# Kernel tuning notes

Measured on AMD Instinct MI355X. Metric: run time of the kernel, lower is better.

Reference implementation:

```python
import jax, jax.numpy as jnp
import numpy as np


def setup_inputs() -> dict:
    key = jax.random.key(0)
    k1, k2, k3, k4 = jax.random.split(key, 4)
    N, T, F = 8192, 128, 9
    M_s = 256
    merged = jax.random.normal(k1, (N, T, F), dtype=jnp.float32)
    input1 = jax.random.normal(k2, (N, T, F), dtype=jnp.float32)
    samples = jax.random.normal(k3, (N, M_s), dtype=jnp.float32)
    labels = jax.random.randint(k4, (N,), 0, 10, dtype=jnp.int32)
    return {"merged": merged, "input1": input1, "samples": samples, "labels": labels}


def reference(merged, input1, samples, labels):
    # Pairwise squared distances S_ij = sum_k (s_i - s_j)^2 / M_s, computed via
    # the Gram-matrix identity instead of materializing the [N, N, M_s] tensor.
    M_s = samples.shape[1]
    sq = jnp.sum(samples * samples, axis=-1)                 # [N]
    gram = jnp.einsum('im,jm->ij', samples, samples)         # [N, N]
    S_ij = (sq[:, None] + sq[None, :] - 2.0 * gram) / jnp.float32(M_s)
    same = (labels[:, None] == labels[None, :]).astype(jnp.float32)
    term2 = jnp.mean(jnp.maximum(0.0, (1.0 - same) * (1.0 - S_ij)))
    L_label = 10.0 * jnp.mean(same * S_ij) + 10.0 * term2
    return L_label
```

## Files before the change

kernel.cpp:

```cpp
#include <hip/hip_runtime.h>
#include <hip/hip_bf16.h>

#define NROWS 8192
#define KDIM  256
#define NT    64
#define NBLK  (NT * (NT + 1) / 2)
#define GRID  256

typedef __attribute__((ext_vector_type(4))) float f32x4;

#define GLD(gp, lp)                                                            \
  __builtin_amdgcn_global_load_lds(                                            \
      (const __attribute__((address_space(1))) void*)(gp),                     \
      (__attribute__((address_space(3))) void*)(lp), 16, 0, 0)

__global__ void prep_kernel(const float* __restrict__ samples,
                            unsigned char* __restrict__ sf8,
                            float* __restrict__ sq,
                            float* __restrict__ accg) {
  int row = blockIdx.x, t = threadIdx.x;
  float2 v2 = ((const float2*)samples)[(size_t)row * 128 + t];
  int pk = __builtin_amdgcn_cvt_pk_fp8_f32(v2.x, v2.y, 0, false);
  ((unsigned short*)sf8)[(size_t)row * 128 + t] = (unsigned short)(pk & 0xffff);
  float p = v2.x * v2.x + v2.y * v2.y;
#pragma unroll
  for (int off = 32; off; off >>= 1) p += __shfl_down(p, off);
  __shared__ float ws2[2];
  if ((t & 63) == 0) ws2[t >> 6] = p;
  __syncthreads();
  if (t == 0) sq[row] = ws2[0] + ws2[1];
  if (row == 0 && t < 2) accg[t] = 0.0f;
}

__device__ inline void decode_tile(int b, int& bi, int& bj) {
  float disc = (2.0f * NT + 1.0f) * (2.0f * NT + 1.0f) - 8.0f * (float)b;
  bi = (int)(((2.0f * NT + 1.0f) - sqrtf(disc)) * 0.5f);
  if (bi < 0) bi = 0;
  if (bi > NT - 1) bi = NT - 1;
  while (bi > 0 && (bi * NT - bi * (bi - 1) / 2) > b) --bi;
  while (((bi + 1) * NT - (bi + 1) * bi / 2) <= b) ++bi;
  bj = bi + (b - (bi * NT - bi * (bi - 1) / 2));
}

__global__ __launch_bounds__(512, 1) void pair_kernel(
    const unsigned char* __restrict__ sf8, const float* __restrict__ sq,
    const int* __restrict__ labels, float* __restrict__ accg) {

  __shared__ __align__(16) unsigned char As[2][128 * 256];
  __shared__ __align__(16) unsigned char Bs[2][128 * 256];
  __shared__ float red[16];

  int t = threadIdx.x;
  int lane = t & 63;
  int w = t >> 6;
  int wm = w >> 1, wn = w & 1;
  int lr = lane >> 4, pc = lane & 15;
  int r = lane & 15;
  int kq = (lane >> 4) >> 1;
  int hf = ((lane >> 4) & 1) * 8;
  int q4 = (lane >> 4) * 4;
  int cl = lane & 15;

  float s1t = 0.f, s2t = 0.f;

  auto stage = [&](int bi_, int bj_, int buf) {
    int rA = bi_ * 128, rB = bj_ * 128;
#pragma unroll
    for (int p = 0; p < 4; ++p) {
      int region = p * 8 + w;
      int rr = region * 4 + lr;
      int c = pc ^ (rr & 15);
      GLD(sf8 + (size_t)(rA + rr) * KDIM + c * 16, &As[buf][region * 1024]);
      GLD(sf8 + (size_t)(rB + rr) * KDIM + c * 16, &Bs[buf][region * 1024]);
    }
  };

  int tile = blockIdx.x;
  int bi, bj;
  decode_tile(tile, bi, bj);
  stage(bi, bj, 0);
  int cur = 0;

  while (tile < NBLK) {
    int ntile = tile + GRID;
    int nbi = 0, nbj = 0;
    bool have_next = ntile < NBLK;
    if (have_next) decode_tile(ntile, nbi, nbj);

    __syncthreads();

    int rowA0 = bi * 128, rowB0 = bj * 128;
    float sqa[8], sqb[4];
    int laa[8], lab[4];
#pragma unroll
    for (int i = 0; i < 2; i++)
#pragma unroll
      for (int q = 0; q < 4; q++) {
        int gr = rowA0 + wm * 32 + i * 16 + q4 + q;
        sqa[i * 4 + q] = sq[gr];
        laa[i * 4 + q] = labels[gr];
      }
#pragma unroll
    for (int j = 0; j < 4; j++) {
      int gc = rowB0 + wn * 64 + j * 16 + cl;
      sqb[j] = sq[gc];
      lab[j] = labels[gc];
    }

    if (have_next) stage(nbi, nbj, cur ^ 1);

    f32x4 acc[2][4];
#pragma unroll
    for (int i = 0; i < 2; i++)
#pragma unroll
      for (int j = 0; j < 4; j++) acc[i][j] = (f32x4){0.f, 0.f, 0.f, 0.f};

#pragma unroll
    for (int kc = 0; kc < 8; ++kc) {
      long af[2], bfr[4];
#pragma unroll
      for (int i = 0; i < 2; i++) {
        int m = wm * 32 + i * 16 + r;
        af[i] = *(const long*)(&As[cur][m * 256 + (((kc * 2 + kq) ^ r) * 16) + hf]);
      }
#pragma unroll
      for (int j = 0; j < 4; j++) {
        int n = wn * 64 + j * 16 + r;
        bfr[j] = *(const long*)(&Bs[cur][n * 256 + (((kc * 2 + kq) ^ r) * 16) + hf]);
      }
#pragma unroll
      for (int i = 0; i < 2; i++)
#pragma unroll
        for (int j = 0; j < 4; j++)
          acc[i][j] = __builtin_amdgcn_mfma_f32_16x16x32_fp8_fp8(
              af[i], bfr[j], acc[i][j], 0, 0, 0);
    }

    float s1 = 0.f, s2 = 0.f;
#pragma unroll
    for (int j = 0; j < 4; j++) {
#pragma unroll
      for (int i = 0; i < 2; i++) {
#pragma unroll
        for (int q = 0; q < 4; q++) {
          float S = (sqa[i * 4 + q] + sqb[j] - 2.0f * acc[i][j][q]) *
                    (1.0f / 256.0f);
          if (laa[i * 4 + q] == lab[j]) s1 += S;
          else                          s2 += fmaxf(0.f, 1.f - S);
        }
      }
    }
    float wt = (bi == bj) ? 1.0f : 2.0f;
    s1t += wt * s1;
    s2t += wt * s2;

    tile = ntile; bi = nbi; bj = nbj; cur ^= 1;
  }

#pragma unroll
  for (int off = 32; off; off >>= 1) {
    s1t += __shfl_down(s1t, off);
    s2t += __shfl_down(s2t, off);
  }
  if (lane == 0) { red[w] = s1t; red[8 + w] = s2t; }
  __syncthreads();
  if (t == 0) {
    float a = 0.f, b2 = 0.f;
#pragma unroll
    for (int k = 0; k < 8; k++) { a += red[k]; b2 += red[8 + k]; }
    atomicAdd(&accg[0], a);
    atomicAdd(&accg[1], b2);
  }
}

__global__ void finalize_kernel(const float* __restrict__ accg,
                                float* __restrict__ out) {
  out[0] = 10.0f * (accg[0] + accg[1]) *
           (1.0f / ((float)NROWS * (float)NROWS));
}

extern "C" void kernel_launch(void* const* d_in, const int* in_sizes, int n_in,
                              void* d_out, int out_size, void* d_ws,
                              size_t ws_size, hipStream_t stream) {
  const float* samples = (const float*)d_in[2];
  const int*   labels  = (const int*)d_in[3];

  char* ws = (char*)d_ws;
  unsigned char* sf8 = (unsigned char*)ws;
  float* sq   = (float*)(ws + (size_t)NROWS * KDIM);
  float* accg = (float*)(ws + (size_t)NROWS * KDIM + NROWS * 4);
  float* out  = (float*)d_out;

  prep_kernel<<<NROWS, 128, 0, stream>>>(samples, sf8, sq, accg);
  pair_kernel<<<GRID, 512, 0, stream>>>(sf8, sq, labels, accg);
  finalize_kernel<<<1, 1, 0, stream>>>(accg, out);
}
```

Baseline: 136.4 us.

## Switch to 32x32x64 scaled FP8 MFMA with packed row metadata

Replaces the 16x16x32 FP8 MFMA tiles with the gfx950 32x32x64 scaled f8f6f4 MFMA, so each wave issues fewer, larger matrix instructions with 128-bit LDS fragment loads. Squared norms (prescaled by 1/256) and labels are packed into a float2 metadata array in the prep kernel, which cuts the scattered scalar loads in the epilogue. The two loss accumulators are merged into one select-based sum. The accumulator layout changes, so correctness depends on the new lane-to-element mapping being right.

```diff
diff --git a/kernel.cpp b/kernel.cpp
--- a/kernel.cpp
+++ b/kernel.cpp
@@ -1,5 +1,4 @@
 #include <hip/hip_runtime.h>
-#include <hip/hip_bf16.h>
 
 #define NROWS 8192
 #define KDIM  256
@@ -7,7 +6,10 @@
 #define NBLK  (NT * (NT + 1) / 2)
 #define GRID  256
 
-typedef __attribute__((ext_vector_type(4))) float f32x4;
+typedef __attribute__((ext_vector_type(4)))  float f32x4;
+typedef __attribute__((ext_vector_type(16))) float f32x16;
+typedef __attribute__((ext_vector_type(4)))  int   i32x4;
+typedef __attribute__((ext_vector_type(8)))  int   i32x8;
 
 #define GLD(gp, lp)                                                            \
   __builtin_amdgcn_global_load_lds(                                            \
@@ -15,8 +17,9 @@
       (__attribute__((address_space(3))) void*)(lp), 16, 0, 0)
 
 __global__ void prep_kernel(const float* __restrict__ samples,
+                            const int* __restrict__ labels,
                             unsigned char* __restrict__ sf8,
-                            float* __restrict__ sq,
+                            float2* __restrict__ meta,
                             float* __restrict__ accg) {
   int row = blockIdx.x, t = threadIdx.x;
   float2 v2 = ((const float2*)samples)[(size_t)row * 128 + t];
@@ -28,7 +31,10 @@
   __shared__ float ws2[2];
   if ((t & 63) == 0) ws2[t >> 6] = p;
   __syncthreads();
-  if (t == 0) sq[row] = ws2[0] + ws2[1];
+  if (t == 0) {
+    float tot = ws2[0] + ws2[1];
+    meta[row] = make_float2(tot * (1.0f / 256.0f), (float)labels[row]);
+  }
   if (row == 0 && t < 2) accg[t] = 0.0f;
 }
 
@@ -43,25 +49,22 @@
 }
 
 __global__ __launch_bounds__(512, 1) void pair_kernel(
-    const unsigned char* __restrict__ sf8, const float* __restrict__ sq,
-    const int* __restrict__ labels, float* __restrict__ accg) {
+    const unsigned char* __restrict__ sf8, const float2* __restrict__ meta,
+    float* __restrict__ accg) {
 
   __shared__ __align__(16) unsigned char As[2][128 * 256];
   __shared__ __align__(16) unsigned char Bs[2][128 * 256];
-  __shared__ float red[16];
+  __shared__ float red[8];
 
   int t = threadIdx.x;
   int lane = t & 63;
   int w = t >> 6;
   int wm = w >> 1, wn = w & 1;
   int lr = lane >> 4, pc = lane & 15;
-  int r = lane & 15;
-  int kq = (lane >> 4) >> 1;
-  int hf = ((lane >> 4) & 1) * 8;
-  int q4 = (lane >> 4) * 4;
-  int cl = lane & 15;
+  int l31 = lane & 31;
+  int hk  = lane >> 5;
 
-  float s1t = 0.f, s2t = 0.f;
+  float stt = 0.f;
 
   auto stage = [&](int bi_, int bj_, int buf) {
     int rA = bi_ * 128, rB = bj_ * 128;
@@ -90,93 +93,84 @@
     __syncthreads();
 
     int rowA0 = bi * 128, rowB0 = bj * 128;
-    float sqa[8], sqb[4];
-    int laa[8], lab[4];
+    float sqa_s[16], laaf[16];
 #pragma unroll
-    for (int i = 0; i < 2; i++)
+    for (int g = 0; g < 4; ++g) {
+      int gr = rowA0 + wm * 32 + g * 8 + 4 * hk;
+      f32x4 m0 = *(const f32x4*)(meta + gr);
+      f32x4 m1 = *(const f32x4*)(meta + gr + 2);
+      sqa_s[g * 4 + 0] = m0.x; laaf[g * 4 + 0] = m0.y;
+      sqa_s[g * 4 + 1] = m0.z; laaf[g * 4 + 1] = m0.w;
+      sqa_s[g * 4 + 2] = m1.x; laaf[g * 4 + 2] = m1.y;
+      sqa_s[g * 4 + 3] = m1.z; laaf[g * 4 + 3] = m1.w;
+    }
+    float sqb_s[2], labf[2];
 #pragma unroll
-      for (int q = 0; q < 4; q++) {
-        int gr = rowA0 + wm * 32 + i * 16 + q4 + q;
-        sqa[i * 4 + q] = sq[gr];
-        laa[i * 4 + q] = labels[gr];
-      }
-#pragma unroll
-    for (int j = 0; j < 4; j++) {
-      int gc = rowB0 + wn * 64 + j * 16 + cl;
-      sqb[j] = sq[gc];
-      lab[j] = labels[gc];
+    for (int j = 0; j < 2; ++j) {
+      float2 mb = meta[rowB0 + wn * 64 + j * 32 + l31];
+      sqb_s[j] = mb.x; labf[j] = mb.y;
     }
 
     if (have_next) stage(nbi, nbj, cur ^ 1);
 
-    f32x4 acc[2][4];
+    f32x16 acc[2];
 #pragma unroll
-    for (int i = 0; i < 2; i++)
+    for (int j = 0; j < 2; ++j)
 #pragma unroll
-      for (int j = 0; j < 4; j++) acc[i][j] = (f32x4){0.f, 0.f, 0.f, 0.f};
+      for (int e = 0; e < 16; ++e) acc[j][e] = 0.f;
 
 #pragma unroll
-    for (int kc = 0; kc < 8; ++kc) {
-      long af[2], bfr[4];
+    for (int kt = 0; kt < 4; ++kt) {
+      int c0 = kt * 4 + hk * 2;
+      int m = wm * 32 + l31;
+      const unsigned char* ab = &As[cur][m * 256];
+      int sm = m & 15;
+      i32x4 alo = *(const i32x4*)(ab + ((c0 ^ sm) << 4));
+      i32x4 ahi = *(const i32x4*)(ab + (((c0 + 1) ^ sm) << 4));
+      i32x8 av = {alo.x, alo.y, alo.z, alo.w, ahi.x, ahi.y, ahi.z, ahi.w};
 #pragma unroll
-      for (int i = 0; i < 2; i++) {
-        int m = wm * 32 + i * 16 + r;
-        af[i] = *(const long*)(&As[cur][m * 256 + (((kc * 2 + kq) ^ r) * 16) + hf]);
+      for (int j = 0; j < 2; ++j) {
+        int n = wn * 64 + j * 32 + l31;
+        const unsigned char* bb = &Bs[cur][n * 256];
+        int sn = n & 15;
+        i32x4 blo = *(const i32x4*)(bb + ((c0 ^ sn) << 4));
+        i32x4 bhi = *(const i32x4*)(bb + (((c0 + 1) ^ sn) << 4));
+        i32x8 bv = {blo.x, blo.y, blo.z, blo.w, bhi.x, bhi.y, bhi.z, bhi.w};
+        acc[j] = __builtin_amdgcn_mfma_scale_f32_32x32x64_f8f6f4(
+            av, bv, acc[j], 0, 0, 0, 127, 0, 127);
       }
-#pragma unroll
-      for (int j = 0; j < 4; j++) {
-        int n = wn * 64 + j * 16 + r;
-        bfr[j] = *(const long*)(&Bs[cur][n * 256 + (((kc * 2 + kq) ^ r) * 16) + hf]);
-      }
-#pragma unroll
-      for (int i = 0; i < 2; i++)
-#pragma unroll
-        for (int j = 0; j < 4; j++)
-          acc[i][j] = __builtin_amdgcn_mfma_f32_16x16x32_fp8_fp8(
-              af[i], bfr[j], acc[i][j], 0, 0, 0);
     }
 
-    float s1 = 0.f, s2 = 0.f;
+    float s = 0.f;
 #pragma unroll
-    for (int j = 0; j < 4; j++) {
+    for (int j = 0; j < 2; ++j) {
 #pragma unroll
-      for (int i = 0; i < 2; i++) {
-#pragma unroll
-        for (int q = 0; q < 4; q++) {
-          float S = (sqa[i * 4 + q] + sqb[j] - 2.0f * acc[i][j][q]) *
-                    (1.0f / 256.0f);
-          if (laa[i * 4 + q] == lab[j]) s1 += S;
-          else                          s2 += fmaxf(0.f, 1.f - S);
-        }
+      for (int g2 = 0; g2 < 16; ++g2) {
+        float S = sqa_s[g2] + sqb_s[j] - acc[j][g2] * (1.0f / 128.0f);
+        float h = fmaxf(0.f, 1.f - S);
+        s += (laaf[g2] == labf[j]) ? S : h;
       }
     }
-    float wt = (bi == bj) ? 1.0f : 2.0f;
-    s1t += wt * s1;
-    s2t += wt * s2;
+    stt += ((bi == bj) ? 1.0f : 2.0f) * s;
 
     tile = ntile; bi = nbi; bj = nbj; cur ^= 1;
   }
 
 #pragma unroll
-  for (int off = 32; off; off >>= 1) {
-    s1t += __shfl_down(s1t, off);
-    s2t += __shfl_down(s2t, off);
-  }
-  if (lane == 0) { red[w] = s1t; red[8 + w] = s2t; }
+  for (int off = 32; off; off >>= 1) stt += __shfl_down(stt, off);
+  if (lane == 0) red[w] = stt;
   __syncthreads();
   if (t == 0) {
-    float a = 0.f, b2 = 0.f;
+    float a = 0.f;
 #pragma unroll
-    for (int k = 0; k < 8; k++) { a += red[k]; b2 += red[8 + k]; }
+    for (int k = 0; k < 8; k++) a += red[k];
     atomicAdd(&accg[0], a);
-    atomicAdd(&accg[1], b2);
   }
 }
 
 __global__ void finalize_kernel(const float* __restrict__ accg,
                                 float* __restrict__ out) {
-  out[0] = 10.0f * (accg[0] + accg[1]) *
-           (1.0f / ((float)NROWS * (float)NROWS));
+  out[0] = 10.0f * accg[0] * (1.0f / ((float)NROWS * (float)NROWS));
 }
 
 extern "C" void kernel_launch(void* const* d_in, const int* in_sizes, int n_in,
@@ -187,11 +181,11 @@
 
   char* ws = (char*)d_ws;
   unsigned char* sf8 = (unsigned char*)ws;
-  float* sq   = (float*)(ws + (size_t)NROWS * KDIM);
-  float* accg = (float*)(ws + (size_t)NROWS * KDIM + NROWS * 4);
-  float* out  = (float*)d_out;
+  float2* meta = (float2*)(ws + (size_t)NROWS * KDIM);
+  float* accg  = (float*)(ws + (size_t)NROWS * KDIM + NROWS * 8);
+  float* out   = (float*)d_out;
 
-  prep_kernel<<<NROWS, 128, 0, stream>>>(samples, sf8, sq, accg);
-  pair_kernel<<<GRID, 512, 0, stream>>>(sf8, sq, labels, accg);
+  prep_kernel<<<NROWS, 128, 0, stream>>>(samples, labels, sf8, meta, accg);
+  pair_kernel<<<GRID, 512, 0, stream>>>(sf8, meta, accg);
   finalize_kernel<<<1, 1, 0, stream>>>(accg, out);
 }
```

New measurement: 124.6 us. 1.09x faster.
